# Performance work log

Measured on AMD Instinct MI355X. Metric: run time of the kernel, lower is better.

Reference implementation:

```python
import jax, jax.numpy as jnp
import numpy as np
from math import log

T, B, IN, H1, H2, OUT = 128, 256, 1024, 2048, 2048, 512
DT, INIT_TAU, MIN_TAU, THRESH, VREST = 0.01, 0.5, 0.1, 1.0, 0.0
SLOPE = 25.0  # snntorch surrogate.fast_sigmoid default slope

@jax.custom_vjp
def spike_fn(x):
    # Heaviside forward; fast-sigmoid surrogate backward
    return (x > 0).astype(x.dtype)

def _spike_fwd(x):
    return spike_fn(x), x

def _spike_bwd(x, g):
    return (g / (SLOPE * jnp.abs(x) + 1.0) ** 2,)

spike_fn.defvjp(_spike_fwd, _spike_bwd)

def setup_inputs() -> dict:
    key = jax.random.key(0)
    ks = jax.random.split(key, 7)
    init_w = -log(1.0 / (INIT_TAU - MIN_TAU) - 1.0)
    def lin(k, fan_in, fan_out):
        bound = 1.0 / np.sqrt(fan_in)
        kw, kb = jax.random.split(k)
        W = jax.random.uniform(kw, (fan_out, fan_in), jnp.float32, -bound, bound)
        b = jax.random.uniform(kb, (fan_out,), jnp.float32, -bound, bound)
        return W, b
    W1, b1 = lin(ks[0], IN, H1)
    W2, b2 = lin(ks[1], H1, H2)
    W3, b3 = lin(ks[2], H2, OUT)
    s = (jax.random.uniform(ks[3], (T, B, IN), jnp.float32) < 0.2).astype(jnp.float32)
    return {
        "s": s,
        "W1": W1, "b1": b1, "wt1": jnp.full((H1,), init_w, jnp.float32),
        "W2": W2, "b2": b2, "wt2": jnp.full((H2,), init_w, jnp.float32),
        "W3": W3, "b3": b3, "wt3": jnp.full((OUT,), init_w, jnp.float32),
    }

def _lif(v, cur, w_tau):
    tau = MIN_TAU + jax.nn.sigmoid(w_tau)
    v = v + (DT / tau) * (-(v - VREST) + cur)  # r = 1.0
    spike = spike_fn(v - THRESH)
    v_post = v * (1.0 - spike)  # zero reset
    return v_post, spike, v  # v is pre-reset membrane (v_tmp)

def reference(s, W1, b1, wt1, W2, b2, wt2, W3, b3, wt3):
    v0 = (jnp.zeros((B, H1), s.dtype), jnp.zeros((B, H2), s.dtype), jnp.zeros((B, OUT), s.dtype))
    def step(carry, st):
        v1, v2, v3 = carry
        v1, s1, _ = _lif(v1, st @ W1.T + b1, wt1)
        v2, s2, _ = _lif(v2, s1 @ W2.T + b2, wt2)
        v3, s3, vtmp = _lif(v3, s2 @ W3.T + b3, wt3)
        return (v1, v2, v3), (s3, vtmp)
    _, (out_s, out_v) = jax.lax.scan(step, v0, s)
    return out_s, out_v
```

## Files before the change

### kernel.cpp

```cpp
#include <hip/hip_runtime.h>
#include <hip/hip_bf16.h>
#include <cstdint>
#include <cstddef>

#define T_STEPS 128
#define BATCH   256
#define IN_F    1024
#define H1_F    2048
#define H2_F    2048
#define OUT_F   512
#define M_TOT   (T_STEPS * BATCH)

#define W1_SCALE 4064.0f
#define W1_INV   (1.0f / 4064.0f)

#define S_F4_BLOCKS 8192
#define W_F4_BLOCKS 512

typedef __attribute__((ext_vector_type(4))) int   int4v;
typedef __attribute__((ext_vector_type(8))) unsigned short ushort8;
typedef unsigned long long ull;

__device__ __forceinline__ void load16_to_lds(const void* g, void* l) {
  __builtin_amdgcn_global_load_lds(
      (const __attribute__((address_space(1))) void*)g,
      (__attribute__((address_space(3))) void*)l, 16, 0, 0);
}

__device__ __forceinline__ unsigned short f2bf(float x) {
  __hip_bfloat16 h = __float2bfloat16(x);
  return *reinterpret_cast<unsigned short*>(&h);
}

__device__ __forceinline__ float bf2f(unsigned short u) {
  unsigned int w = ((unsigned int)u) << 16;
  return *reinterpret_cast<float*>(&w);
}

__device__ __forceinline__ float lif_k(float w) {
  float tau = 0.1f + 1.0f / (1.0f + expf(-w));
  return 0.01f / tau;
}

__global__ __launch_bounds__(256) void cvt_both(
    const float4* __restrict__ s_in, unsigned int* __restrict__ s_out,
    const float4* __restrict__ w_in, unsigned int* __restrict__ w_out) {
  const int tid = threadIdx.x, lane = tid & 63, wv = tid >> 6;
  const int bid = blockIdx.x;
  const bool is_s = bid < S_F4_BLOCKS;
  const float4* in;
  unsigned int* out;
  size_t base;
  if (is_s) {
    in = s_in; out = s_out;
    base = (size_t)bid * 1024 + wv * 256 + lane;
  } else {
    in = w_in; out = w_out;
    base = (size_t)(bid - S_F4_BLOCKS) * 1024 + wv * 256 + lane;
  }
#pragma unroll
  for (int q = 0; q < 4; ++q) {
    float4 v = in[base + q * 64];
    unsigned int p;
    if (is_s) {
      p = (v.x > 0.5f ? 1u : 0u) | (v.y > 0.5f ? 0x100u : 0u) |
          (v.z > 0.5f ? 0x10000u : 0u) | (v.w > 0.5f ? 0x1000000u : 0u);
    } else {
      int c0 = __float2int_rn(v.x * W1_SCALE), c1 = __float2int_rn(v.y * W1_SCALE);
      int c2 = __float2int_rn(v.z * W1_SCALE), c3 = __float2int_rn(v.w * W1_SCALE);
      p = (c0 & 0xff) | ((c1 & 0xff) << 8) | ((c2 & 0xff) << 16) | ((c3 & 0xff) << 24);
    }
    out[base + q * 64] = p;
  }
}

union SMem {
  struct { uint4 lA[1024]; uint4 lB[1024]; } st;
  unsigned short tile[128 * 136];
};

__global__ __launch_bounds__(256) void gemm_scan(
    const int8_t* __restrict__ A, const int8_t* __restrict__ B,
    const float* __restrict__ b1, const float* __restrict__ wt1,
    ull* __restrict__ mask1) {
  __shared__ SMem sm;
  const int K = IN_F;
  const int tid = threadIdx.x, lane = tid & 63, wv = tid >> 6;
  const int wm = (wv & 1) * 64, wn = (wv >> 1) * 64;

  const int id = blockIdx.x;
  const int xcd = id & 7, j = id >> 3;
  const int bblk = xcd * 32 + (j >> 4);
  const int n0   = (j & 15) * 128;

  const int mk = lane & 15, grp = lane >> 4;

  int4v acc[4][4] = {};

  for (int kt = 0; kt < K; kt += 128) {
#pragma unroll
    for (int i = 0; i < 4; ++i) {
      int cellbase = (wv * 4 + i) * 64;
      int cell = cellbase + lane;
      int r  = cell >> 3;
      int kb = (cell & 7) ^ (r & 7);
      load16_to_lds(A + (size_t)(r * BATCH + bblk) * K + kt + kb * 16, &sm.st.lA[cellbase]);
      load16_to_lds(B + (size_t)(n0 + r) * K + kt + kb * 16, &sm.st.lB[cellbase]);
    }
    __syncthreads();
#pragma unroll
    for (int ks = 0; ks < 2; ++ks) {
      int4v af[4], bfr[4];
      const int kb = ks * 4 + grp;
#pragma unroll
      for (int f = 0; f < 4; ++f) {
        int m = wm + f * 16 + mk;
        af[f]  = *(const int4v*)&sm.st.lA[m * 8 + (kb ^ (m & 7))];
        int n = wn + f * 16 + mk;
        bfr[f] = *(const int4v*)&sm.st.lB[n * 8 + (kb ^ (n & 7))];
      }
#pragma unroll
      for (int i = 0; i < 4; ++i)
#pragma unroll
        for (int jj = 0; jj < 4; ++jj)
          acc[i][jj] = __builtin_amdgcn_mfma_i32_16x16x64_i8(af[i], bfr[jj], acc[i][jj], 0, 0, 0);
    }
    __syncthreads();
  }

#pragma unroll
  for (int jj = 0; jj < 4; ++jj) {
    const int h = wn + jj * 16 + mk;
#pragma unroll
    for (int i = 0; i < 4; ++i) {
      const int t0 = wm + i * 16 + grp * 4;
      uint2 pk;
      pk.x = ((unsigned int)f2bf((float)acc[i][jj][1] * W1_INV) << 16)
           | f2bf((float)acc[i][jj][0] * W1_INV);
      pk.y = ((unsigned int)f2bf((float)acc[i][jj][3] * W1_INV) << 16)
           | f2bf((float)acc[i][jj][2] * W1_INV);
      *(uint2*)&sm.tile[h * 136 + t0] = pk;
    }
  }
  __syncthreads();

  if (tid < 128) {
    const int h  = tid;
    const int hg = n0 + h;
    const int wv2 = tid >> 6;
    const int ln  = tid & 63;
    const float bias = b1[hg];
    const float k    = lif_k(wt1[hg]);
    const size_t wbase = (size_t)(n0 >> 6) + wv2;
    float v = 0.0f;
    for (int t8 = 0; t8 < T_STEPS; t8 += 8) {
      ushort8 pk = *(const ushort8*)&sm.tile[h * 136 + t8];
#pragma unroll
      for (int u = 0; u < 8; ++u) {
        v = fmaf(k, (bf2f(pk[u]) + bias) - v, v);
        bool sp = v > 1.0f;
        ull bm = __ballot(sp);
        if (ln == 0)
          mask1[((size_t)(t8 + u) * BATCH + bblk) * (H1_F / 64) + wbase] = bm;
        if (sp) v = 0.0f;
      }
    }
  }
}

__global__ __launch_bounds__(1024) void layer23_kernel(
    const ull* __restrict__ mask1,
    const float* __restrict__ W2, const float* __restrict__ b2, const float* __restrict__ wt2,
    const float* __restrict__ W3, const float* __restrict__ b3, const float* __restrict__ wt3,
    float* __restrict__ out_s, float* __restrict__ out_v) {
  __shared__ ull m1all[T_STEPS * 32];
  __shared__ ull m2sh[2][32];
  const int tid = threadIdx.x, b = blockIdx.x;
  const int lane = tid & 63, wv = tid >> 6;

  const float bias2a = b2[tid], bias2b = b2[tid + 1024];
  const float k2a = lif_k(wt2[tid]), k2b = lif_k(wt2[tid + 1024]);
  const float* W2a = W2 + (size_t)tid * H1_F;
  const float* W2b = W2 + (size_t)(tid + 1024) * H1_F;
  float v2a = 0.0f, v2b = 0.0f;

  float bias3 = 0.0f, k3 = 0.0f, v3 = 0.0f;
  const float* W3r = W3;
  if (wv < 8) {
    bias3 = b3[tid];
    k3 = lif_k(wt3[tid]);
    W3r = W3 + (size_t)tid * H2_F;
  }

#pragma unroll
  for (int u = 0; u < 4; ++u) {
    int idx = tid + u * 1024;
    m1all[idx] = mask1[((size_t)(idx >> 5) * BATCH + b) * 32 + (idx & 31)];
  }
  __syncthreads();

  for (int t = 0; t < T_STEPS; ++t) {
    ull wrd = (lane < 32) ? m1all[t * 32 + lane] : 0ull;

    float cura = bias2a, curb = bias2b;
    if (__ballot(wrd != 0ull)) {
      for (int wi = 0; wi < 32; ++wi) {
        ull m = __shfl(wrd, wi, 64);
        while (m) {
          int bit = __ffsll(m) - 1;
          m &= m - 1;
          int idx = wi * 64 + bit;
          cura += W2a[idx];
          curb += W2b[idx];
        }
      }
    }
    v2a = fmaf(k2a, cura - v2a, v2a);
    v2b = fmaf(k2b, curb - v2b, v2b);
    bool spa = v2a > 1.0f, spb = v2b > 1.0f;
    ull sa = __ballot(spa);
    ull sb = __ballot(spb);
    if (lane == 0) { m2sh[t & 1][wv] = sa; m2sh[t & 1][16 + wv] = sb; }
    if (spa) v2a = 0.0f;
    if (spb) v2b = 0.0f;
    __syncthreads();

    if (wv < 8) {
      ull w3m = (lane < 32) ? m2sh[t & 1][lane] : 0ull;
      float cur3 = bias3;
      if (__ballot(w3m != 0ull)) {
        for (int wi = 0; wi < 32; ++wi) {
          ull m = __shfl(w3m, wi, 64);
          while (m) {
            int bit = __ffsll(m) - 1;
            m &= m - 1;
            cur3 += W3r[wi * 64 + bit];
          }
        }
      }
      float vp = fmaf(k3, cur3 - v3, v3);
      bool sp = vp > 1.0f;
      size_t idx = (size_t)(t * BATCH + b) * OUT_F + tid;
      out_s[idx] = sp ? 1.0f : 0.0f;
      out_v[idx] = vp;
      v3 = sp ? 0.0f : vp;
    }
  }
}

extern "C" void kernel_launch(void* const* d_in, const int* in_sizes, int n_in,
                              void* d_out, int out_size, void* d_ws, size_t ws_size,
                              hipStream_t stream) {
  const float* s   = (const float*)d_in[0];
  const float* W1  = (const float*)d_in[1];
  const float* b1  = (const float*)d_in[2];
  const float* wt1 = (const float*)d_in[3];
  const float* W2  = (const float*)d_in[4];
  const float* b2  = (const float*)d_in[5];
  const float* wt2 = (const float*)d_in[6];
  const float* W3  = (const float*)d_in[7];
  const float* b3  = (const float*)d_in[8];
  const float* wt3 = (const float*)d_in[9];

  char* wsb = (char*)d_ws;
  const size_t MASK_BYTES = (size_t)T_STEPS * BATCH * (H1_F / 64) * 8;
  const size_t S_ELEMS  = (size_t)M_TOT * IN_F;
  ull* mask1 = (ull*)wsb;
  int8_t* s_i8  = (int8_t*)(wsb + MASK_BYTES);
  int8_t* W1_i8 = s_i8 + S_ELEMS;
  (void)ws_size;

  float* outs = (float*)d_out;
  float* outv = outs + (size_t)T_STEPS * BATCH * OUT_F;

  cvt_both<<<S_F4_BLOCKS + W_F4_BLOCKS, 256, 0, stream>>>(
      (const float4*)s, (unsigned int*)s_i8, (const float4*)W1, (unsigned int*)W1_i8);

  gemm_scan<<<BATCH * (H1_F / 128), 256, 0, stream>>>(s_i8, W1_i8, b1, wt1, mask1);

  layer23_kernel<<<BATCH, 1024, 0, stream>>>(mask1, W2, b2, wt2, W3, b3, wt3, outs, outv);
}
```

Before: 379.6 us.

## Load GEMM operands directly from global into registers with prefetch, drop LDS staging

Replaces the LDS-staged int8 GEMM main loop, which used global_load_lds plus two barriers per k-tile, with direct per-lane 16-byte global loads into MFMA operand registers. It is fully unrolled over K with one-step register double buffering. The aim is to remove LDS traffic and synchronisation. In exchange each wave refetches A and B rows that other waves also use, which raises global/L2 traffic, and the row-strided 16-byte loads coalesce worse.

After: 529.3 us. +39.5%, slower.

```diff
diff --git a/kernel.cpp b/kernel.cpp
--- a/kernel.cpp
+++ b/kernel.cpp
@@ -20,12 +20,6 @@
 typedef __attribute__((ext_vector_type(4))) int   int4v;
 typedef __attribute__((ext_vector_type(8))) unsigned short ushort8;
 typedef unsigned long long ull;
-
-__device__ __forceinline__ void load16_to_lds(const void* g, void* l) {
-  __builtin_amdgcn_global_load_lds(
-      (const __attribute__((address_space(1))) void*)g,
-      (__attribute__((address_space(3))) void*)l, 16, 0, 0);
-}
 
 __device__ __forceinline__ unsigned short f2bf(float x) {
   __hip_bfloat16 h = __float2bfloat16(x);
@@ -74,16 +68,11 @@
   }
 }
 
-union SMem {
-  struct { uint4 lA[1024]; uint4 lB[1024]; } st;
-  unsigned short tile[128 * 136];
-};
-
 __global__ __launch_bounds__(256) void gemm_scan(
     const int8_t* __restrict__ A, const int8_t* __restrict__ B,
     const float* __restrict__ b1, const float* __restrict__ wt1,
     ull* __restrict__ mask1) {
-  __shared__ SMem sm;
+  __shared__ unsigned short tile[128 * 136];
   const int K = IN_F;
   const int tid = threadIdx.x, lane = tid & 63, wv = tid >> 6;
   const int wm = (wv & 1) * 64, wn = (wv >> 1) * 64;
@@ -95,38 +84,45 @@
 
   const int mk = lane & 15, grp = lane >> 4;
 
+  const int8_t* ap[4];
+  const int8_t* bp[4];
+#pragma unroll
+  for (int f = 0; f < 4; ++f) {
+    const int m = wm + f * 16 + mk;
+    ap[f] = A + (size_t)(m * BATCH + bblk) * K + grp * 16;
+    const int n = n0 + wn + f * 16 + mk;
+    bp[f] = B + (size_t)n * K + grp * 16;
+  }
+
   int4v acc[4][4] = {};
-
-  for (int kt = 0; kt < K; kt += 128) {
-#pragma unroll
-    for (int i = 0; i < 4; ++i) {
-      int cellbase = (wv * 4 + i) * 64;
-      int cell = cellbase + lane;
-      int r  = cell >> 3;
-      int kb = (cell & 7) ^ (r & 7);
-      load16_to_lds(A + (size_t)(r * BATCH + bblk) * K + kt + kb * 16, &sm.st.lA[cellbase]);
-      load16_to_lds(B + (size_t)(n0 + r) * K + kt + kb * 16, &sm.st.lB[cellbase]);
-    }
-    __syncthreads();
-#pragma unroll
-    for (int ks = 0; ks < 2; ++ks) {
-      int4v af[4], bfr[4];
-      const int kb = ks * 4 + grp;
-#pragma unroll
-      for (int f = 0; f < 4; ++f) {
-        int m = wm + f * 16 + mk;
-        af[f]  = *(const int4v*)&sm.st.lA[m * 8 + (kb ^ (m & 7))];
-        int n = wn + f * 16 + mk;
-        bfr[f] = *(const int4v*)&sm.st.lB[n * 8 + (kb ^ (n & 7))];
-      }
-#pragma unroll
-      for (int i = 0; i < 4; ++i)
-#pragma unroll
-        for (int jj = 0; jj < 4; ++jj)
-          acc[i][jj] = __builtin_amdgcn_mfma_i32_16x16x64_i8(af[i], bfr[jj], acc[i][jj], 0, 0, 0);
-    }
-    __syncthreads();
-  }
+  int4v a_cur[4], b_cur[4];
+#pragma unroll
+  for (int f = 0; f < 4; ++f) {
+    a_cur[f] = *(const int4v*)(ap[f]);
+    b_cur[f] = *(const int4v*)(bp[f]);
+  }
+
+#pragma unroll
+  for (int s = 1; s < 16; ++s) {
+    int4v a_nxt[4], b_nxt[4];
+#pragma unroll
+    for (int f = 0; f < 4; ++f) {
+      a_nxt[f] = *(const int4v*)(ap[f] + s * 64);
+      b_nxt[f] = *(const int4v*)(bp[f] + s * 64);
+    }
+#pragma unroll
+    for (int i = 0; i < 4; ++i)
+#pragma unroll
+      for (int jj = 0; jj < 4; ++jj)
+        acc[i][jj] = __builtin_amdgcn_mfma_i32_16x16x64_i8(a_cur[i], b_cur[jj], acc[i][jj], 0, 0, 0);
+#pragma unroll
+    for (int f = 0; f < 4; ++f) { a_cur[f] = a_nxt[f]; b_cur[f] = b_nxt[f]; }
+  }
+#pragma unroll
+  for (int i = 0; i < 4; ++i)
+#pragma unroll
+    for (int jj = 0; jj < 4; ++jj)
+      acc[i][jj] = __builtin_amdgcn_mfma_i32_16x16x64_i8(a_cur[i], b_cur[jj], acc[i][jj], 0, 0, 0);
 
 #pragma unroll
   for (int jj = 0; jj < 4; ++jj) {
@@ -139,7 +135,7 @@
            | f2bf((float)acc[i][jj][0] * W1_INV);
       pk.y = ((unsigned int)f2bf((float)acc[i][jj][3] * W1_INV) << 16)
            | f2bf((float)acc[i][jj][2] * W1_INV);
-      *(uint2*)&sm.tile[h * 136 + t0] = pk;
+      *(uint2*)&tile[h * 136 + t0] = pk;
     }
   }
   __syncthreads();
@@ -154,7 +150,7 @@
     const size_t wbase = (size_t)(n0 >> 6) + wv2;
     float v = 0.0f;
     for (int t8 = 0; t8 < T_STEPS; t8 += 8) {
-      ushort8 pk = *(const ushort8*)&sm.tile[h * 136 + t8];
+      ushort8 pk = *(const ushort8*)&tile[h * 136 + t8];
 #pragma unroll
       for (int u = 0; u < 8; ++u) {
         v = fmaf(k, (bf2f(pk[u]) + bias) - v, v);
```
